# Optimization experiments

Hardware: AMD Instinct MI355X
Metric: run time of the kernel (lower is better)

## Reference

```python
import jax, jax.numpy as jnp
import numpy as np

N_NODES = 50000
D_FEAT = 512
H1, H2 = 128, 64
N_CLASSES = 40
E_MP = 800000
E_LP = 250000


def gcn_conv(x, W, b, edge_index, edge_weight, num_nodes):
    """PyG GCNConv: add self-loops, symmetric norm D^-1/2 (A+I) D^-1/2, then (norm-agg)(xW)+b."""
    row, col = edge_index[0], edge_index[1]
    loop = jnp.arange(num_nodes)
    row = jnp.concatenate([row, loop])
    col = jnp.concatenate([col, loop])
    ew = jnp.concatenate([edge_weight, jnp.ones((num_nodes,), x.dtype)])
    deg = jax.ops.segment_sum(ew, col, num_segments=num_nodes)
    dinv = jnp.where(deg > 0, deg ** -0.5, 0.0).astype(x.dtype)
    norm = dinv[row] * ew * dinv[col]  # [E+N]
    h = x @ W  # [N, out]
    msg = h[row] * norm[:, None]  # gather + scale per edge
    out = jax.ops.segment_sum(msg, col, num_segments=num_nodes) + b
    return out


def setup_inputs() -> dict:
    key = jax.random.key(0)
    ks = jax.random.split(key, 16)
    inp = {}
    inp["x"] = jax.random.normal(ks[0], (N_NODES, D_FEAT), jnp.float32)
    inp["train_pos_edge_index"] = jax.random.randint(ks[1], (2, E_MP), 0, N_NODES)
    inp["edge_index"] = jax.random.randint(ks[2], (2, E_MP), 0, N_NODES)
    inp["edge_weight"] = jax.random.uniform(ks[3], (E_MP,), jnp.float32)
    inp["pos_edge_index"] = jax.random.randint(ks[4], (2, E_LP), 0, N_NODES)
    inp["neg_edge_index"] = jax.random.randint(ks[5], (2, E_LP), 0, N_NODES)
    # parameters (glorot-ish scaled)
    def w(k, i, o):
        return jax.random.normal(k, (i, o), jnp.float32) * (2.0 / (i + o)) ** 0.5
    inp["W1"] = w(ks[6], D_FEAT, H1)
    inp["b1"] = jnp.zeros((H1,), jnp.float32)
    inp["W2"] = w(ks[7], H1, H2)
    inp["b2"] = jnp.zeros((H2,), jnp.float32)
    inp["W_attr"] = w(ks[8], H2, N_CLASSES)
    inp["b_attr"] = jnp.zeros((N_CLASSES,), jnp.float32)
    inp["W_att"] = w(ks[9], H2, N_CLASSES)
    inp["b_att"] = jnp.zeros((N_CLASSES,), jnp.float32)
    return inp


def reference(x, train_pos_edge_index, edge_index, edge_weight, pos_edge_index,
              neg_edge_index, W1, b1, W2, b2, W_attr, b_attr, W_att, b_att):
    ones = jnp.ones((train_pos_edge_index.shape[1],), x.dtype)
    h = jax.nn.relu(gcn_conv(x, W1, b1, train_pos_edge_index, ones, N_NODES))
    h = gcn_conv(h, W2, b2, train_pos_edge_index, ones, N_NODES)  # [N, 64]
    attr = gcn_conv(h, W_attr, b_attr, edge_index, edge_weight, N_NODES)
    # gradient reversal is identity in forward
    att = gcn_conv(h, W_att, b_att, edge_index, edge_weight, N_NODES)
    total = jnp.concatenate([pos_edge_index, neg_edge_index], axis=-1)  # [2, 2*E_LP]
    x_j = h[total[0]]
    x_i = h[total[1]]
    res = jnp.einsum("ef,ef->e", x_i, x_j)
    return res, jax.nn.log_softmax(attr, axis=1), jax.nn.log_softmax(att, axis=1)
```

## Files before the change

kernel.cpp:

```cpp
#include <hip/hip_runtime.h>

typedef short s16x8 __attribute__((ext_vector_type(8)));
typedef short s16x4 __attribute__((ext_vector_type(4)));
typedef float f32x4 __attribute__((ext_vector_type(4)));

static __device__ __forceinline__ unsigned short f2bf(float f) {
  unsigned u = __float_as_uint(f);
  u += 0x7fff + ((u >> 16) & 1);
  return (unsigned short)(u >> 16);
}
static __device__ __forceinline__ float bf2f(unsigned short h) {
  return __uint_as_float(((unsigned)h) << 16);
}


static __global__ void k_init(int* cntT, int* cntE, int n) {
  int i = blockIdx.x * blockDim.x + threadIdx.x;
  if (i < n) { cntT[i] = 0; cntE[i] = 0; }
}

static __global__ void k_count(const int* __restrict__ tcol, const int* __restrict__ ecol,
                               int* __restrict__ cntT, int* __restrict__ cntE,
                               int* __restrict__ rankT, int* __restrict__ rankE, int E) {
  int base = (blockIdx.x * blockDim.x + threadIdx.x) * 4;
  if (base + 3 < E) {
    int4 tc = *(const int4*)&tcol[base];
    int4 ec = *(const int4*)&ecol[base];
    int4 rt, re;
    rt.x = atomicAdd(&cntT[tc.x], 1);
    rt.y = atomicAdd(&cntT[tc.y], 1);
    rt.z = atomicAdd(&cntT[tc.z], 1);
    rt.w = atomicAdd(&cntT[tc.w], 1);
    re.x = atomicAdd(&cntE[ec.x], 1);
    re.y = atomicAdd(&cntE[ec.y], 1);
    re.z = atomicAdd(&cntE[ec.z], 1);
    re.w = atomicAdd(&cntE[ec.w], 1);
    *(int4*)&rankT[base] = rt;
    *(int4*)&rankE[base] = re;
  } else {
    for (int e = base; e < E; ++e) {
      rankT[e] = atomicAdd(&cntT[tcol[e]], 1);
      rankE[e] = atomicAdd(&cntE[ecol[e]], 1);
    }
  }
}

static __global__ __launch_bounds__(256) void k_scanA(
    const int* __restrict__ cntT, const int* __restrict__ cntE,
    int* __restrict__ bsum, int n, int nb) {
  const int* cnt = blockIdx.y ? cntE : cntT;
  int tid = threadIdx.x;
  int base = blockIdx.x * 1024 + tid * 4;
  int s = 0;
#pragma unroll
  for (int q = 0; q < 4; ++q) { int i = base + q; if (i < n) s += cnt[i]; }
  __shared__ int red[256];
  red[tid] = s;
  __syncthreads();
  for (int off = 128; off > 0; off >>= 1) {
    if (tid < off) red[tid] += red[tid + off];
    __syncthreads();
  }
  if (tid == 0) bsum[blockIdx.y * nb + blockIdx.x] = red[0];
}

static __global__ void k_scanB(int* bsum, int* ptrT, int* ptrE, int nb, int n) {
  int a = threadIdx.x;
  if (a > 1) return;
  int* bs = bsum + a * nb;
  int run = 0;
  for (int i = 0; i < nb; ++i) { int c = bs[i]; bs[i] = run; run += c; }
  (a ? ptrE : ptrT)[n] = run;
}

static __global__ __launch_bounds__(256) void k_scanC(
    const int* __restrict__ cntT, const int* __restrict__ cntE,
    const int* __restrict__ bsum, int* __restrict__ ptrT, int* __restrict__ ptrE,
    int n, int nb) {
  const int* cnt = blockIdx.y ? cntE : cntT;
  int* ptr = blockIdx.y ? ptrE : ptrT;
  int tid = threadIdx.x;
  int pre = bsum[blockIdx.y * nb + blockIdx.x];
  int base = blockIdx.x * 1024 + tid * 4;
  int v[4];
  int s = 0;
#pragma unroll
  for (int q = 0; q < 4; ++q) { int i = base + q; v[q] = (i < n) ? cnt[i] : 0; s += v[q]; }
  __shared__ int red[256];
  red[tid] = s;
  __syncthreads();
  for (int off = 1; off < 256; off <<= 1) {
    int t = (tid >= off) ? red[tid - off] : 0;
    __syncthreads();
    red[tid] += t;
    __syncthreads();
  }
  int run = pre + (tid ? red[tid - 1] : 0);
#pragma unroll
  for (int q = 0; q < 4; ++q) {
    int i = base + q;
    if (i < n) ptr[i] = run;
    run += v[q];
  }
}

static __global__ void k_fill(const int* __restrict__ trow, const int* __restrict__ tcol,
                              const int* __restrict__ erow, const int* __restrict__ ecol,
                              const float* __restrict__ ew,
                              const int* __restrict__ ptrT, const int* __restrict__ ptrE,
                              const int* __restrict__ rankT, const int* __restrict__ rankE,
                              int* __restrict__ srcT, int2* __restrict__ srcwE, int E) {
  int base = (blockIdx.x * blockDim.x + threadIdx.x) * 4;
  if (base + 3 < E) {
    int4 tr = *(const int4*)&trow[base];
    int4 tc = *(const int4*)&tcol[base];
    int4 er = *(const int4*)&erow[base];
    int4 ec = *(const int4*)&ecol[base];
    float4 w = *(const float4*)&ew[base];
    int4 rt = *(const int4*)&rankT[base];
    int4 re = *(const int4*)&rankE[base];
    srcT[ptrT[tc.x] + rt.x] = tr.x;
    srcT[ptrT[tc.y] + rt.y] = tr.y;
    srcT[ptrT[tc.z] + rt.z] = tr.z;
    srcT[ptrT[tc.w] + rt.w] = tr.w;
    int2 p;
    p.x = er.x; p.y = __float_as_int(w.x); srcwE[ptrE[ec.x] + re.x] = p;
    p.x = er.y; p.y = __float_as_int(w.y); srcwE[ptrE[ec.y] + re.y] = p;
    p.x = er.z; p.y = __float_as_int(w.z); srcwE[ptrE[ec.z] + re.z] = p;
    p.x = er.w; p.y = __float_as_int(w.w); srcwE[ptrE[ec.w] + re.w] = p;
  } else {
    for (int e = base; e < E; ++e) {
      srcT[ptrT[tcol[e]] + rankT[e]] = trow[e];
      int2 p;
      p.x = erow[e];
      p.y = __float_as_int(ew[e]);
      srcwE[ptrE[ecol[e]] + rankE[e]] = p;
    }
  }
}

static __global__ void k_dinv2(const int* __restrict__ cntT, const int2* __restrict__ srcwE,
                               const int* __restrict__ ptrE,
                               float* __restrict__ dinvT, float* __restrict__ dinvE, int n) {
  int i = blockIdx.x * blockDim.x + threadIdx.x;
  if (i >= n) return;
  dinvT[i] = rsqrtf((float)cntT[i] + 1.0f);
  float s = 1.0f;
  int e = ptrE[i + 1];
  for (int j = ptrE[i]; j < e; ++j) s += __int_as_float(srcwE[j].y);
  dinvE[i] = rsqrtf(s);
}


static __global__ void k_cvtW(const float* __restrict__ W, unsigned short* __restrict__ Wh,
                              unsigned short* __restrict__ Wl, int K, int Nc) {
  int t = blockIdx.x * blockDim.x + threadIdx.x;
  if (t >= K * Nc) return;
  int k = t / Nc, c = t - k * Nc;
  float v = W[t];
  unsigned short hi = f2bf(v);
  size_t o = (size_t)(k >> 5) * (Nc * 32) + c * 32 + (k & 31);
  Wh[o] = hi;
  Wl[o] = f2bf(v - bf2f(hi));
}


#define PADU 36
#define GK 512
#define NKT 16

static __global__ __launch_bounds__(256) void k_gemm_mfma_split(
    const float* __restrict__ A, const unsigned short* __restrict__ Bh,
    const unsigned short* __restrict__ Bl, float* __restrict__ C, int M) {
  __shared__ __align__(16) unsigned short Ah[2][64][PADU];
  __shared__ __align__(16) unsigned short Al[2][64][PADU];
  int tid = threadIdx.x;
  int lane = tid & 63, wid = tid >> 6;
  int wr = wid >> 1, wc = wid & 1;
  int l15 = lane & 15, l4 = lane >> 4;
  int brow = blockIdx.x * 64;
  f32x4 acc[2][4] = {};

  int ar = tid >> 3, ac4 = (tid & 7) * 4;
  int ar2 = (tid + 256) >> 3, ac42 = ((tid + 256) & 7) * 4;
  const float* Arow1 = &A[(size_t)min(brow + ar, M - 1) * GK + ac4];
  const float* Arow2 = &A[(size_t)min(brow + ar2, M - 1) * GK + ac42];
  bool v1ok = (brow + ar < M), v2ok = (brow + ar2 < M);

  float4 v[2];
  s16x8 bhc[4], blc[4], bhn[4], bln[4];
  size_t boff = (size_t)(wc * 64 + l15) * 32 + l4 * 8;

  v[0] = v1ok ? *(const float4*)Arow1 : make_float4(0.f, 0.f, 0.f, 0.f);
  v[1] = v2ok ? *(const float4*)Arow2 : make_float4(0.f, 0.f, 0.f, 0.f);
#pragma unroll
  for (int n = 0; n < 4; ++n) {
    bhc[n] = *(const s16x8*)&Bh[boff + n * 512];
    blc[n] = *(const s16x8*)&Bl[boff + n * 512];
  }
  {
    float4 w0 = v[0], w1 = v[1];
    unsigned short h;
    s16x4 hv, lv;
    h = f2bf(w0.x); hv[0] = h; lv[0] = (short)f2bf(w0.x - bf2f(h));
    h = f2bf(w0.y); hv[1] = h; lv[1] = (short)f2bf(w0.y - bf2f(h));
    h = f2bf(w0.z); hv[2] = h; lv[2] = (short)f2bf(w0.z - bf2f(h));
    h = f2bf(w0.w); hv[3] = h; lv[3] = (short)f2bf(w0.w - bf2f(h));
    *(s16x4*)&Ah[0][ar][ac4] = hv;
    *(s16x4*)&Al[0][ar][ac4] = lv;
    h = f2bf(w1.x); hv[0] = h; lv[0] = (short)f2bf(w1.x - bf2f(h));
    h = f2bf(w1.y); hv[1] = h; lv[1] = (short)f2bf(w1.y - bf2f(h));
    h = f2bf(w1.z); hv[2] = h; lv[2] = (short)f2bf(w1.z - bf2f(h));
    h = f2bf(w1.w); hv[3] = h; lv[3] = (short)f2bf(w1.w - bf2f(h));
    *(s16x4*)&Ah[0][ar2][ac42] = hv;
    *(s16x4*)&Al[0][ar2][ac42] = lv;
  }
  v[0] = v1ok ? *(const float4*)(Arow1 + 32) : make_float4(0.f, 0.f, 0.f, 0.f);
  v[1] = v2ok ? *(const float4*)(Arow2 + 32) : make_float4(0.f, 0.f, 0.f, 0.f);
#pragma unroll
  for (int n = 0; n < 4; ++n) {
    bhn[n] = *(const s16x8*)&Bh[4096 + boff + n * 512];
    bln[n] = *(const s16x8*)&Bl[4096 + boff + n * 512];
  }
  __syncthreads();

#pragma unroll
  for (int kt = 0; kt < NKT; ++kt) {
    int S = kt & 1;
    s16x8 afh[2], afl[2];
#pragma unroll
    for (int m = 0; m < 2; ++m) {
      int r = wr * 32 + m * 16 + l15;
      afh[m] = *(const s16x8*)&Ah[S][r][l4 * 8];
      afl[m] = *(const s16x8*)&Al[S][r][l4 * 8];
    }
    if (kt + 1 < NKT) {
      float4 w0 = v[0], w1 = v[1];
      unsigned short h;
      s16x4 hv, lv;
      h = f2bf(w0.x); hv[0] = h; lv[0] = (short)f2bf(w0.x - bf2f(h));
      h = f2bf(w0.y); hv[1] = h; lv[1] = (short)f2bf(w0.y - bf2f(h));
      h = f2bf(w0.z); hv[2] = h; lv[2] = (short)f2bf(w0.z - bf2f(h));
      h = f2bf(w0.w); hv[3] = h; lv[3] = (short)f2bf(w0.w - bf2f(h));
      *(s16x4*)&Ah[S ^ 1][ar][ac4] = hv;
      *(s16x4*)&Al[S ^ 1][ar][ac4] = lv;
      h = f2bf(w1.x); hv[0] = h; lv[0] = (short)f2bf(w1.x - bf2f(h));
      h = f2bf(w1.y); hv[1] = h; lv[1] = (short)f2bf(w1.y - bf2f(h));
      h = f2bf(w1.z); hv[2] = h; lv[2] = (short)f2bf(w1.z - bf2f(h));
      h = f2bf(w1.w); hv[3] = h; lv[3] = (short)f2bf(w1.w - bf2f(h));
      *(s16x4*)&Ah[S ^ 1][ar2][ac42] = hv;
      *(s16x4*)&Al[S ^ 1][ar2][ac42] = lv;
      if (kt + 2 < NKT) {
        v[0] = v1ok ? *(const float4*)(Arow1 + (kt + 2) * 32) : make_float4(0.f, 0.f, 0.f, 0.f);
        v[1] = v2ok ? *(const float4*)(Arow2 + (kt + 2) * 32) : make_float4(0.f, 0.f, 0.f, 0.f);
      }
    }
#pragma unroll
    for (int m = 0; m < 2; ++m)
#pragma unroll
      for (int n = 0; n < 4; ++n) {
        acc[m][n] = __builtin_amdgcn_mfma_f32_16x16x32_bf16(afh[m], bhc[n], acc[m][n], 0, 0, 0);
        acc[m][n] = __builtin_amdgcn_mfma_f32_16x16x32_bf16(afl[m], bhc[n], acc[m][n], 0, 0, 0);
        acc[m][n] = __builtin_amdgcn_mfma_f32_16x16x32_bf16(afh[m], blc[n], acc[m][n], 0, 0, 0);
      }
    if (kt + 1 < NKT) {
#pragma unroll
      for (int n = 0; n < 4; ++n) { bhc[n] = bhn[n]; blc[n] = bln[n]; }
      if (kt + 2 < NKT) {
        size_t o = (size_t)(kt + 2) * 4096 + boff;
#pragma unroll
        for (int n = 0; n < 4; ++n) {
          bhn[n] = *(const s16x8*)&Bh[o + n * 512];
          bln[n] = *(const s16x8*)&Bl[o + n * 512];
        }
      }
      __syncthreads();
    }
  }

#pragma unroll
  for (int m = 0; m < 2; ++m) {
    int rbase = brow + wr * 32 + m * 16 + l4 * 4;
#pragma unroll
    for (int n = 0; n < 4; ++n) {
      int c = wc * 64 + n * 16 + l15;
#pragma unroll
      for (int j = 0; j < 4; ++j) {
        int r = rbase + j;
        if (r < M) C[(size_t)r * 128 + c] = acc[m][n][j];
      }
    }
  }
}


template <int F, bool RELU, bool WEIGHTED>
static __global__ __launch_bounds__(256) void k_gather4(
    const float* __restrict__ H, const int* __restrict__ rowptr,
    const int* __restrict__ src, const int2* __restrict__ srcw,
    const float* __restrict__ dinv, const float* __restrict__ Hpre,
    const float* __restrict__ bias, float* __restrict__ out, int n) {
  const int L = F / 4;
  int node = blockIdx.x * (256 / L) + threadIdx.x / L;
  if (node >= n) return;
  int f4 = (threadIdx.x % L) * 4;
  float d = dinv[node];
  float4 hp = *(const float4*)&Hpre[(size_t)node * F + f4];
  float ax = hp.x * d, ay = hp.y * d, az = hp.z * d, aw = hp.w * d;
  int j = rowptr[node], e = rowptr[node + 1];
  for (; j + 1 < e; j += 2) {
    int r0, r1;
    float w0, w1;
    if (WEIGHTED) {
      int2 a = srcw[j], b = srcw[j + 1];
      r0 = a.x; r1 = b.x;
      w0 = dinv[r0] * __int_as_float(a.y);
      w1 = dinv[r1] * __int_as_float(b.y);
    } else {
      r0 = src[j]; r1 = src[j + 1];
      w0 = dinv[r0]; w1 = dinv[r1];
    }
    float4 v0 = *(const float4*)&H[(size_t)r0 * F + f4];
    float4 v1 = *(const float4*)&H[(size_t)r1 * F + f4];
    ax += v0.x * w0 + v1.x * w1;
    ay += v0.y * w0 + v1.y * w1;
    az += v0.z * w0 + v1.z * w1;
    aw += v0.w * w0 + v1.w * w1;
  }
  if (j < e) {
    int r;
    float wj;
    if (WEIGHTED) { int2 a = srcw[j]; r = a.x; wj = dinv[r] * __int_as_float(a.y); }
    else { r = src[j]; wj = dinv[r]; }
    float4 v = *(const float4*)&H[(size_t)r * F + f4];
    ax += v.x * wj; ay += v.y * wj; az += v.z * wj; aw += v.w * wj;
  }
  float bx = 0, by = 0, bz = 0, bw = 0;
  if (bias) { float4 bb = *(const float4*)&bias[f4]; bx = bb.x; by = bb.y; bz = bb.z; bw = bb.w; }
  ax = ax * d + bx; ay = ay * d + by; az = az * d + bz; aw = aw * d + bw;
  if (RELU) { ax = fmaxf(ax, 0.f); ay = fmaxf(ay, 0.f); az = fmaxf(az, 0.f); aw = fmaxf(aw, 0.f); }
  float4 o; o.x = ax; o.y = ay; o.z = az; o.w = aw;
  *(float4*)&out[(size_t)node * F + f4] = o;
}


static __global__ __launch_bounds__(256) void k_gemm(
    const float* __restrict__ A, const float* __restrict__ B,
    const float* __restrict__ bias, float* __restrict__ C,
    int M, int N, int K) {
  const int BM = 64, BN = 64, BK = 16;
  __shared__ float As[BK][BM + 4];
  __shared__ float Bs[BK][BN + 4];
  int tid = threadIdx.x;
  int tr = tid >> 4, tc = tid & 15;
  int brow = blockIdx.y * BM, bcol = blockIdx.x * BN;
  float acc[4][4] = {};
  for (int k0 = 0; k0 < K; k0 += BK) {
#pragma unroll
    for (int i = tid; i < BM * BK; i += 256) {
      int m = i >> 4, kk = i & 15;
      int gr = brow + m;
      As[kk][m] = (gr < M) ? A[(size_t)gr * K + k0 + kk] : 0.f;
    }
#pragma unroll
    for (int i = tid; i < BK * BN; i += 256) {
      int kk = i >> 6, n = i & 63;
      int gc = bcol + n;
      Bs[kk][n] = (gc < N) ? B[(size_t)(k0 + kk) * N + gc] : 0.f;
    }
    __syncthreads();
#pragma unroll
    for (int kk = 0; kk < BK; ++kk) {
      float a[4], b[4];
#pragma unroll
      for (int i = 0; i < 4; ++i) a[i] = As[kk][tr * 4 + i];
#pragma unroll
      for (int j = 0; j < 4; ++j) b[j] = Bs[kk][tc * 4 + j];
#pragma unroll
      for (int i = 0; i < 4; ++i)
#pragma unroll
        for (int j = 0; j < 4; ++j) acc[i][j] += a[i] * b[j];
    }
    __syncthreads();
  }
#pragma unroll
  for (int i = 0; i < 4; ++i) {
    int r = brow + tr * 4 + i;
    if (r >= M) continue;
#pragma unroll
    for (int j = 0; j < 4; ++j) {
      int c = bcol + tc * 4 + j;
      if (c < N) C[(size_t)r * N + c] = acc[i][j] + (bias ? bias[c] : 0.f);
    }
  }
}


static __global__ void k_logsoftmax40(float* __restrict__ X, int n) {
  int i = blockIdx.x * blockDim.x + threadIdx.x;
  if (i >= n) return;
  float4 v[10];
#pragma unroll
  for (int q = 0; q < 10; ++q) v[q] = *(const float4*)&X[(size_t)i * 40 + q * 4];
  float m = -1e30f;
#pragma unroll
  for (int q = 0; q < 10; ++q)
    m = fmaxf(m, fmaxf(fmaxf(v[q].x, v[q].y), fmaxf(v[q].z, v[q].w)));
  float s = 0.f;
#pragma unroll
  for (int q = 0; q < 10; ++q)
    s += expf(v[q].x - m) + expf(v[q].y - m) + expf(v[q].z - m) + expf(v[q].w - m);
  float ls = logf(s) + m;
#pragma unroll
  for (int q = 0; q < 10; ++q) {
    float4 o; o.x = v[q].x - ls; o.y = v[q].y - ls; o.z = v[q].z - ls; o.w = v[q].w - ls;
    *(float4*)&X[(size_t)i * 40 + q * 4] = o;
  }
}


static __global__ __launch_bounds__(256) void k_linkpred4(
    const float* __restrict__ H2, const int* __restrict__ pos,
    const int* __restrict__ neg, float* __restrict__ res, int Elp) {
  int t = blockIdx.x * 256 + threadIdx.x;
  int e = t >> 4, f4 = (t & 15) * 4;
  if (e >= 2 * Elp) return;
  int a, b;
  if (e < Elp) { a = pos[e]; b = pos[Elp + e]; }
  else { int e2 = e - Elp; a = neg[e2]; b = neg[Elp + e2]; }
  float4 va = *(const float4*)&H2[(size_t)a * 64 + f4];
  float4 vb = *(const float4*)&H2[(size_t)b * 64 + f4];
  float p = va.x * vb.x + va.y * vb.y + va.z * vb.z + va.w * vb.w;
  p += __shfl_xor(p, 1);
  p += __shfl_xor(p, 2);
  p += __shfl_xor(p, 4);
  p += __shfl_xor(p, 8);
  if ((t & 15) == 0) res[e] = p;
}


extern "C" void kernel_launch(void* const* d_in, const int* in_sizes, int n_in,
                              void* d_out, int out_size, void* d_ws, size_t ws_size,
                              hipStream_t stream) {
  const float* x    = (const float*)d_in[0];
  const int*   tp   = (const int*)d_in[1];
  const int*   ei   = (const int*)d_in[2];
  const float* ew   = (const float*)d_in[3];
  const int*   pos  = (const int*)d_in[4];
  const int*   neg  = (const int*)d_in[5];
  const float* W1   = (const float*)d_in[6];
  const float* b1   = (const float*)d_in[7];
  const float* W2   = (const float*)d_in[8];
  const float* b2   = (const float*)d_in[9];
  const float* Wattr= (const float*)d_in[10];
  const float* battr= (const float*)d_in[11];
  const float* Watt = (const float*)d_in[12];
  const float* batt = (const float*)d_in[13];

  const int N   = in_sizes[0] / 512;
  const int EMP = in_sizes[1] / 2;
  const int ELP = in_sizes[4] / 2;
  const int NB  = (N + 1023) / 1024;

  float* ws = (float*)d_ws;
  float* dinvT = ws;
  float* dinvE = dinvT + N;
  int* rowptrT = (int*)(dinvE + N);
  int* rowptrE = rowptrT + (N + 4);
  int* srcT    = rowptrE + (N + 4);
  int2* srcwE  = (int2*)(srcT + EMP);
  int* bsum    = (int*)(srcwE + EMP);
  unsigned short* W1h = (unsigned short*)(bsum + 128);
  unsigned short* W1l = W1h + 512 * 128;
  float* bufA  = (float*)(W1l + 512 * 128);
  float* bufB  = bufA + (size_t)N * 128;
  float* bufC  = bufB + (size_t)N * 128;
  int* rankT = (int*)bufA;
  int* rankE = rankT + EMP;
  int* cntT  = (int*)bufB;
  int* cntE  = cntT + N;

  float* out_res  = (float*)d_out;
  float* out_attr = out_res + 2 * (size_t)ELP;
  float* out_att  = out_attr + (size_t)N * 40;

  dim3 b256(256);
  int gN = (N + 255) / 256;
  int gE4 = (EMP + 1023) / 1024;

  k_init<<<gN, b256, 0, stream>>>(cntT, cntE, N);
  k_cvtW<<<(512 * 128 + 255) / 256, b256, 0, stream>>>(W1, W1h, W1l, 512, 128);
  k_count<<<gE4, b256, 0, stream>>>(tp + EMP, ei + EMP, cntT, cntE, rankT, rankE, EMP);
  {
    dim3 gs(NB, 2);
    k_scanA<<<gs, b256, 0, stream>>>(cntT, cntE, bsum, N, NB);
    k_scanB<<<1, 64, 0, stream>>>(bsum, rowptrT, rowptrE, NB, N);
    k_scanC<<<gs, b256, 0, stream>>>(cntT, cntE, bsum, rowptrT, rowptrE, N, NB);
  }
  k_fill<<<gE4, b256, 0, stream>>>(tp, tp + EMP, ei, ei + EMP, ew,
                                   rowptrT, rowptrE, rankT, rankE, srcT, srcwE, EMP);
  k_dinv2<<<gN, b256, 0, stream>>>(cntT, srcwE, rowptrE, dinvT, dinvE, N);

  k_gemm_mfma_split<<<(N + 63) / 64, b256, 0, stream>>>(x, W1h, W1l, bufA, N);
  k_gather4<128, true, false><<<(N + 7) / 8, b256, 0, stream>>>(
      bufA, rowptrT, srcT, nullptr, dinvT, bufA, b1, bufB, N);

  {
    dim3 grid(1, (N + 63) / 64);
    k_gemm<<<grid, b256, 0, stream>>>(bufB, W2, nullptr, bufA, N, 64, 128);
  }
  k_gather4<64, false, false><<<(N + 15) / 16, b256, 0, stream>>>(
      bufA, rowptrT, srcT, nullptr, dinvT, bufA, b2, bufC, N);

  k_gather4<64, false, true><<<(N + 15) / 16, b256, 0, stream>>>(
      bufC, rowptrE, nullptr, srcwE, dinvE, bufC, nullptr, bufA, N);

  {
    dim3 grid(1, (N + 63) / 64);
    k_gemm<<<grid, b256, 0, stream>>>(bufA, Wattr, battr, out_attr, N, 40, 64);
    k_gemm<<<grid, b256, 0, stream>>>(bufA, Watt, batt, out_att, N, 40, 64);
  }
  k_logsoftmax40<<<gN, b256, 0, stream>>>(out_attr, N);
  k_logsoftmax40<<<gN, b256, 0, stream>>>(out_att, N);

  k_linkpred4<<<(2 * ELP * 16 + 255) / 256, b256, 0, stream>>>(bufC, pos, neg, out_res, ELP);
}
```

Before: 430.4 us.

## Load A fragments directly from global into registers, dropping LDS staging

The GEMM kernel no longer stages converted A tiles through double-buffered shared memory. Each wave now loads its own A fragment straight from global memory and splits it into bf16 hi/lo in registers, with no __syncthreads, and adds an occupancy hint of 2 blocks per CU. The aim is to remove LDS traffic, barriers and register pressure from prefetch buffers. In exchange there is no software prefetch, and each A element is loaded and converted by two waves (wc=0 and wc=1), so redundant global or L2 reads and conversions may expose memory latency.

```diff
diff --git a/kernel.cpp b/kernel.cpp
--- a/kernel.cpp
+++ b/kernel.cpp
@@ -1,7 +1,6 @@
 #include <hip/hip_runtime.h>
 
 typedef short s16x8 __attribute__((ext_vector_type(8)));
-typedef short s16x4 __attribute__((ext_vector_type(4)));
 typedef float f32x4 __attribute__((ext_vector_type(4)));
 
 static __device__ __forceinline__ unsigned short f2bf(float f) {
@@ -165,15 +164,22 @@
 }
 
 
-#define PADU 36
 #define GK 512
 #define NKT 16
 
-static __global__ __launch_bounds__(256) void k_gemm_mfma_split(
+static __device__ __forceinline__ void cvt8(float4 a, float4 b, s16x8& hi, s16x8& lo) {
+  float f[8] = {a.x, a.y, a.z, a.w, b.x, b.y, b.z, b.w};
+#pragma unroll
+  for (int i = 0; i < 8; ++i) {
+    unsigned short h = f2bf(f[i]);
+    hi[i] = (short)h;
+    lo[i] = (short)f2bf(f[i] - bf2f(h));
+  }
+}
+
+static __global__ __launch_bounds__(256, 2) void k_gemm_mfma_split(
     const float* __restrict__ A, const unsigned short* __restrict__ Bh,
     const unsigned short* __restrict__ Bl, float* __restrict__ C, int M) {
-  __shared__ __align__(16) unsigned short Ah[2][64][PADU];
-  __shared__ __align__(16) unsigned short Al[2][64][PADU];
   int tid = threadIdx.x;
   int lane = tid & 63, wid = tid >> 6;
   int wr = wid >> 1, wc = wid & 1;
@@ -181,101 +187,38 @@
   int brow = blockIdx.x * 64;
   f32x4 acc[2][4] = {};
 
-  int ar = tid >> 3, ac4 = (tid & 7) * 4;
-  int ar2 = (tid + 256) >> 3, ac42 = ((tid + 256) & 7) * 4;
-  const float* Arow1 = &A[(size_t)min(brow + ar, M - 1) * GK + ac4];
-  const float* Arow2 = &A[(size_t)min(brow + ar2, M - 1) * GK + ac42];
-  bool v1ok = (brow + ar < M), v2ok = (brow + ar2 < M);
-
-  float4 v[2];
-  s16x8 bhc[4], blc[4], bhn[4], bln[4];
+  const float* arow[2];
+#pragma unroll
+  for (int m = 0; m < 2; ++m) {
+    int r = brow + wr * 32 + m * 16 + l15;
+    arow[m] = &A[(size_t)min(r, M - 1) * GK + l4 * 8];
+  }
   size_t boff = (size_t)(wc * 64 + l15) * 32 + l4 * 8;
 
-  v[0] = v1ok ? *(const float4*)Arow1 : make_float4(0.f, 0.f, 0.f, 0.f);
-  v[1] = v2ok ? *(const float4*)Arow2 : make_float4(0.f, 0.f, 0.f, 0.f);
-#pragma unroll
-  for (int n = 0; n < 4; ++n) {
-    bhc[n] = *(const s16x8*)&Bh[boff + n * 512];
-    blc[n] = *(const s16x8*)&Bl[boff + n * 512];
-  }
-  {
-    float4 w0 = v[0], w1 = v[1];
-    unsigned short h;
-    s16x4 hv, lv;
-    h = f2bf(w0.x); hv[0] = h; lv[0] = (short)f2bf(w0.x - bf2f(h));
-    h = f2bf(w0.y); hv[1] = h; lv[1] = (short)f2bf(w0.y - bf2f(h));
-    h = f2bf(w0.z); hv[2] = h; lv[2] = (short)f2bf(w0.z - bf2f(h));
-    h = f2bf(w0.w); hv[3] = h; lv[3] = (short)f2bf(w0.w - bf2f(h));
-    *(s16x4*)&Ah[0][ar][ac4] = hv;
-    *(s16x4*)&Al[0][ar][ac4] = lv;
-    h = f2bf(w1.x); hv[0] = h; lv[0] = (short)f2bf(w1.x - bf2f(h));
-    h = f2bf(w1.y); hv[1] = h; lv[1] = (short)f2bf(w1.y - bf2f(h));
-    h = f2bf(w1.z); hv[2] = h; lv[2] = (short)f2bf(w1.z - bf2f(h));
-    h = f2bf(w1.w); hv[3] = h; lv[3] = (short)f2bf(w1.w - bf2f(h));
-    *(s16x4*)&Ah[0][ar2][ac42] = hv;
-    *(s16x4*)&Al[0][ar2][ac42] = lv;
-  }
-  v[0] = v1ok ? *(const float4*)(Arow1 + 32) : make_float4(0.f, 0.f, 0.f, 0.f);
-  v[1] = v2ok ? *(const float4*)(Arow2 + 32) : make_float4(0.f, 0.f, 0.f, 0.f);
-#pragma unroll
-  for (int n = 0; n < 4; ++n) {
-    bhn[n] = *(const s16x8*)&Bh[4096 + boff + n * 512];
-    bln[n] = *(const s16x8*)&Bl[4096 + boff + n * 512];
-  }
-  __syncthreads();
-
 #pragma unroll
   for (int kt = 0; kt < NKT; ++kt) {
-    int S = kt & 1;
     s16x8 afh[2], afl[2];
 #pragma unroll
     for (int m = 0; m < 2; ++m) {
-      int r = wr * 32 + m * 16 + l15;
-      afh[m] = *(const s16x8*)&Ah[S][r][l4 * 8];
-      afl[m] = *(const s16x8*)&Al[S][r][l4 * 8];
-    }
-    if (kt + 1 < NKT) {
-      float4 w0 = v[0], w1 = v[1];
-      unsigned short h;
-      s16x4 hv, lv;
-      h = f2bf(w0.x); hv[0] = h; lv[0] = (short)f2bf(w0.x - bf2f(h));
-      h = f2bf(w0.y); hv[1] = h; lv[1] = (short)f2bf(w0.y - bf2f(h));
-      h = f2bf(w0.z); hv[2] = h; lv[2] = (short)f2bf(w0.z - bf2f(h));
-      h = f2bf(w0.w); hv[3] = h; lv[3] = (short)f2bf(w0.w - bf2f(h));
-      *(s16x4*)&Ah[S ^ 1][ar][ac4] = hv;
-      *(s16x4*)&Al[S ^ 1][ar][ac4] = lv;
-      h = f2bf(w1.x); hv[0] = h; lv[0] = (short)f2bf(w1.x - bf2f(h));
-      h = f2bf(w1.y); hv[1] = h; lv[1] = (short)f2bf(w1.y - bf2f(h));
-      h = f2bf(w1.z); hv[2] = h; lv[2] = (short)f2bf(w1.z - bf2f(h));
-      h = f2bf(w1.w); hv[3] = h; lv[3] = (short)f2bf(w1.w - bf2f(h));
-      *(s16x4*)&Ah[S ^ 1][ar2][ac42] = hv;
-      *(s16x4*)&Al[S ^ 1][ar2][ac42] = lv;
-      if (kt + 2 < NKT) {
-        v[0] = v1ok ? *(const float4*)(Arow1 + (kt + 2) * 32) : make_float4(0.f, 0.f, 0.f, 0.f);
-        v[1] = v2ok ? *(const float4*)(Arow2 + (kt + 2) * 32) : make_float4(0.f, 0.f, 0.f, 0.f);
+      float4 a0 = *(const float4*)(arow[m] + kt * 32);
+      float4 a1 = *(const float4*)(arow[m] + kt * 32 + 4);
+      cvt8(a0, a1, afh[m], afl[m]);
+    }
+    s16x8 bh[4], bl[4];
+#pragma unroll
+    for (int n = 0; n < 4; ++n) {
+      size_t o = (size_t)kt * 4096 + boff + n * 512;
+      bh[n] = *(const s16x8*)&Bh[o];
+      bl[n] = *(const s16x8*)&Bl[o];
+    }
+#pragma unroll
+    for (int m = 0; m < 2; ++m)
+#pragma unroll
+      for (int n = 0; n < 4; ++n) {
+        acc[m][n] = __builtin_amdgcn_mfma_f32_16x16x32_bf16(afh[m], bh[n], acc[m][n], 0, 0, 0);
+        acc[m][n] = __builtin_amdgcn_mfma_f32_16x16x32_bf16(afl[m], bh[n], acc[m][n], 0, 0, 0);
+        acc[m][n] = __builtin_amdgcn_mfma_f32_16x16x32_bf16(afh[m], bl[n], acc[m][n], 0, 0, 0);
       }
-    }
-#pragma unroll
-    for (int m = 0; m < 2; ++m)
-#pragma unroll
-      for (int n = 0; n < 4; ++n) {
-        acc[m][n] = __builtin_amdgcn_mfma_f32_16x16x32_bf16(afh[m], bhc[n], acc[m][n], 0, 0, 0);
-        acc[m][n] = __builtin_amdgcn_mfma_f32_16x16x32_bf16(afl[m], bhc[n], acc[m][n], 0, 0, 0);
-        acc[m][n] = __builtin_amdgcn_mfma_f32_16x16x32_bf16(afh[m], blc[n], acc[m][n], 0, 0, 0);
-      }
-    if (kt + 1 < NKT) {
-#pragma unroll
-      for (int n = 0; n < 4; ++n) { bhc[n] = bhn[n]; blc[n] = bln[n]; }
-      if (kt + 2 < NKT) {
-        size_t o = (size_t)(kt + 2) * 4096 + boff;
-#pragma unroll
-        for (int n = 0; n < 4; ++n) {
-          bhn[n] = *(const s16x8*)&Bh[o + n * 512];
-          bln[n] = *(const s16x8*)&Bl[o + n * 512];
-        }
-      }
-      __syncthreads();
-    }
   }
 
 #pragma unroll
```

Result: slower. 454.8 us (+5.7%).
